# Kernel optimization log

Hardware: AMD Instinct MI355X
Metric: run time of the kernel (lower is better)

## Reference

```python
import jax, jax.numpy as jnp
import numpy as np

D_MODEL = 256
N_HEADS = 8
D_FF = 1024
N_LAYERS = 6
INPUT_DIM = 2
EPS = 1e-5  # torch LayerNorm default


def _layer_norm(x, g, b):
    m = jnp.mean(x, axis=-1, keepdims=True)
    v = jnp.mean((x - m) ** 2, axis=-1, keepdims=True)
    return (x - m) / jnp.sqrt(v + EPS) * g + b


def setup_inputs() -> dict:
    key = jax.random.key(0)
    ks = jax.random.split(key, 8)
    f32 = jnp.float32

    def w(k, shape, fan_in):
        return jax.random.normal(k, shape, f32) * (1.0 / np.sqrt(fan_in))

    return {
        "x": jax.random.normal(ks[0], (8, 1024, INPUT_DIM), f32),
        "in_w": w(ks[1], (INPUT_DIM, D_MODEL), INPUT_DIM),
        "in_b": jnp.zeros((D_MODEL,), f32),
        "ln1_g": jnp.ones((D_MODEL,), f32),
        "ln1_b": jnp.zeros((D_MODEL,), f32),
        "qkv_w": w(ks[2], (D_MODEL, 3 * D_MODEL), D_MODEL),
        "qkv_b": jnp.zeros((3 * D_MODEL,), f32),
        "out_w": w(ks[3], (D_MODEL, D_MODEL), D_MODEL),
        "out_b": jnp.zeros((D_MODEL,), f32),
        "lna_g": jnp.ones((D_MODEL,), f32),
        "lna_b": jnp.zeros((D_MODEL,), f32),
        "ln2_g": jnp.ones((D_MODEL,), f32),
        "ln2_b": jnp.zeros((D_MODEL,), f32),
        "ff1_w": w(ks[4], (D_MODEL, D_FF), D_MODEL),
        "ff1_b": jnp.zeros((D_FF,), f32),
        "ff2_w": w(ks[5], (D_FF, D_MODEL), D_FF),
        "ff2_b": jnp.zeros((D_MODEL,), f32),
        "lnf_g": jnp.ones((D_MODEL,), f32),
        "lnf_b": jnp.zeros((D_MODEL,), f32),
    }


def reference(x, in_w, in_b, ln1_g, ln1_b, qkv_w, qkv_b, out_w, out_b,
              lna_g, lna_b, ln2_g, ln2_b, ff1_w, ff1_b, ff2_w, ff2_b,
              lnf_g, lnf_b):
    B, L, _ = x.shape
    dk = D_MODEL // N_HEADS
    scale = 1.0 / np.sqrt(dk)
    top_k = max(1, L // 4)

    # sinusoidal positional encoding [L, D]
    pos = jnp.arange(L, dtype=jnp.float32)[:, None]
    div = jnp.exp(jnp.arange(0, D_MODEL, 2, dtype=jnp.float32)
                  * (-np.log(10000.0) / D_MODEL))
    pe = jnp.zeros((L, D_MODEL), jnp.float32)
    pe = pe.at[:, 0::2].set(jnp.sin(pos * div))
    pe = pe.at[:, 1::2].set(jnp.cos(pos * div))

    h = x @ in_w + in_b + pe[None]  # [B, L, D]

    # VoformerEncoder reuses the SAME layer object -> shared weights, 6 passes
    for _ in range(N_LAYERS):
        # --- self-attention sublayer (pre-norm) ---
        s2 = _layer_norm(h, ln1_g, ln1_b)
        qkv = (s2 @ qkv_w + qkv_b).reshape(B, L, 3, N_HEADS, dk)
        q = qkv[:, :, 0].transpose(0, 2, 1, 3)  # [B, H, L, dk]
        k = qkv[:, :, 1].transpose(0, 2, 1, 3)
        v = qkv[:, :, 2].transpose(0, 2, 1, 3)

        scores = jnp.einsum('bhqd,bhkd->bhqk', q, k) * scale  # [B,H,L,L]
        # ProbSparse: keep only the per-row top-k scores
        thr = jax.lax.top_k(scores, top_k)[0][..., -1:]
        sparse = jnp.where(scores >= thr, scores, -jnp.inf)
        attn = jax.nn.softmax(sparse, axis=-1)
        o = jnp.einsum('bhqk,bhkd->bhqd', attn, v)
        o = o.transpose(0, 2, 1, 3).reshape(B, L, D_MODEL)
        o = o @ out_w + out_b
        # InformerAttention applies its own residual + LayerNorm
        attn_out = _layer_norm(o + s2, lna_g, lna_b)
        h = h + attn_out

        # --- FFN sublayer with Volatilite activation ---
        s2 = _layer_norm(h, ln2_g, ln2_b)
        f = s2 @ ff1_w + ff1_b  # [B, L, d_ff]
        mean_f = jnp.mean(f, axis=1, keepdims=True)
        vol = jnp.sqrt(jnp.mean((mean_f - f) ** 2, axis=1, keepdims=True))
        f = f * vol
        f = f @ ff2_w + ff2_b
        h = h + f

    return _layer_norm(h, lnf_g, lnf_b)
```

## Files before the change

### kernel.cpp

```cpp
#include <hip/hip_runtime.h>
#include <math.h>

#define D_MODEL 256
#define NH 8
#define DFF 1024
#define NLAYERS 6
#define B_ 8
#define L_ 1024
#define NR (B_*L_)
#define TOPK 256
#define LNEPS 1e-5f

typedef __attribute__((ext_vector_type(8))) short bf16x8;
typedef __attribute__((ext_vector_type(4))) float f32x4;

__device__ __forceinline__ float wsum(float v){
  #pragma unroll
  for(int o=32;o>0;o>>=1) v += __shfl_xor(v,o,64);
  return v;
}
__device__ __forceinline__ float wmax(float v){
  #pragma unroll
  for(int o=32;o>0;o>>=1) v = fmaxf(v,__shfl_xor(v,o,64));
  return v;
}
__device__ __forceinline__ short f2bf(float x){
  unsigned u = __float_as_uint(x);
  u += 0x7fffu + ((u>>16)&1u);
  return (short)(u>>16);
}
__device__ __forceinline__ float bf2f(short s){
  return __uint_as_float(((unsigned)(unsigned short)s)<<16);
}
__device__ __forceinline__ void g2l(const short* g, short* l){
  __builtin_amdgcn_global_load_lds(
      (const __attribute__((address_space(1))) unsigned int*)g,
      (__attribute__((address_space(3))) unsigned int*)l,
      16, 0, 0);
}

__global__ __launch_bounds__(256) void embed_kernel(
    const float* __restrict__ x, const float* __restrict__ in_w,
    const float* __restrict__ in_b, float* __restrict__ h)
{
  int tid = blockIdx.x*256 + threadIdx.x;
  int n  = tid >> 6;
  int d0 = (tid & 63) << 2;
  int l  = n & (L_-1);
  float x0 = x[2*n], x1 = x[2*n+1];
  const float kf = -0.07195578415606394f;
  float pe[4];
  #pragma unroll
  for(int ii=0; ii<2; ++ii){
    int i = (d0>>1) + ii;
    float dv  = expf((float)i * kf);
    float ang = (float)l * dv;
    pe[2*ii]   = sinf(ang);
    pe[2*ii+1] = cosf(ang);
  }
  float4 w0 = *(const float4*)(in_w + d0);
  float4 w1 = *(const float4*)(in_w + D_MODEL + d0);
  float4 bb = *(const float4*)(in_b + d0);
  float4 o;
  o.x = x0*w0.x + x1*w1.x + bb.x + pe[0];
  o.y = x0*w0.y + x1*w1.y + bb.y + pe[1];
  o.z = x0*w0.z + x1*w1.z + bb.z + pe[2];
  o.w = x0*w0.w + x1*w1.w + bb.w + pe[3];
  *(float4*)(h + (size_t)n*D_MODEL + d0) = o;
}

__global__ __launch_bounds__(256) void wcvt(
    const float* __restrict__ W, short* __restrict__ WT, int N, int kshift)
{
  int idx = blockIdx.x*256 + threadIdx.x;
  int K = 1<<kshift;
  if (idx >= N*K) return;
  int n = idx >> kshift, k = idx & (K-1);
  WT[idx] = f2bf(W[(size_t)k*N + n]);
}

template<int OM>
__global__ __launch_bounds__(256) void ln_kernel(
    const float* __restrict__ in, const float* __restrict__ g,
    const float* __restrict__ b, float* __restrict__ out,
    short* __restrict__ outb)
{
  int wave = threadIdx.x >> 6, lane = threadIdx.x & 63;
  int row = blockIdx.x*4 + wave;
  float4 v = ((const float4*)(in + (size_t)row*D_MODEL))[lane];
  float s  = v.x+v.y+v.z+v.w;
  float sq = v.x*v.x+v.y*v.y+v.z*v.z+v.w*v.w;
  s = wsum(s); sq = wsum(sq);
  float mean = s*(1.f/D_MODEL);
  float var  = sq*(1.f/D_MODEL) - mean*mean;
  float rstd = 1.f/sqrtf(var + LNEPS);
  float4 gv = ((const float4*)g)[lane];
  float4 bv = ((const float4*)b)[lane];
  float4 o;
  o.x = (v.x-mean)*rstd*gv.x + bv.x;
  o.y = (v.y-mean)*rstd*gv.y + bv.y;
  o.z = (v.z-mean)*rstd*gv.z + bv.z;
  o.w = (v.w-mean)*rstd*gv.w + bv.w;
  if (OM == 0 || OM == 1){
    ((float4*)(out + (size_t)row*D_MODEL))[lane] = o;
  }
  if (OM == 3){
    float4* op = (float4*)(out + (size_t)row*D_MODEL) + lane;
    float4 hv = *op;
    o.x+=hv.x; o.y+=hv.y; o.z+=hv.z; o.w+=hv.w;
    *op = o;
  }
  if (OM == 1 || OM == 2){
    short4 s4; s4.x=f2bf(o.x); s4.y=f2bf(o.y); s4.z=f2bf(o.z); s4.w=f2bf(o.w);
    *(short4*)(outb + (size_t)row*D_MODEL + lane*4) = s4;
  }
}

template<int MODE>
__global__ __launch_bounds__(256) void mfma_gemm(
    const short* __restrict__ A, const short* __restrict__ BT,
    const float* __restrict__ bias, const float* __restrict__ resid,
    float* __restrict__ Cf, short* __restrict__ Cb, short* __restrict__ Vt,
    int N, int K)
{
  __shared__ __align__(16) short As[128*32];
  __shared__ __align__(16) short Bs[64*32];
  const int t = threadIdx.x, wv = t>>6, lane = t&63;
  const int r16 = lane&15, quad = lane>>4;
  const int m0 = blockIdx.y*128, n0 = blockIdx.x*64;
  const int ia0 = wv*128 + lane, ia1 = ia0 + 64;
  const int ib  = wv*64 + lane;
  const short* Ab = A  + (size_t)m0*K;
  const short* Bb = BT + (size_t)n0*K;
  const f32x4 z = {0.f,0.f,0.f,0.f};
  f32x4 acc[2][4];
  #pragma unroll
  for (int i=0;i<2;++i)
    #pragma unroll
    for (int j=0;j<4;++j) acc[i][j] = z;

  for (int k0 = 0; k0 < K; k0 += 32){
    __syncthreads();
    g2l(Ab + (size_t)(ia0>>2)*K + k0 + (ia0&3)*8, As + ia0*8);
    g2l(Ab + (size_t)(ia1>>2)*K + k0 + (ia1&3)*8, As + ia1*8);
    g2l(Bb + (size_t)(ib>>2)*K  + k0 + (ib&3)*8,  Bs + ib*8);
    __syncthreads();
    bf16x8 af0 = *(const bf16x8*)(As + ((wv*32      + r16)*32 + quad*8));
    bf16x8 af1 = *(const bf16x8*)(As + ((wv*32 + 16 + r16)*32 + quad*8));
    bf16x8 bf[4];
    #pragma unroll
    for (int ct=0; ct<4; ++ct)
      bf[ct] = *(const bf16x8*)(Bs + ((ct*16 + r16)*32 + quad*8));
    #pragma unroll
    for (int ct=0; ct<4; ++ct){
      acc[0][ct] = __builtin_amdgcn_mfma_f32_16x16x32_bf16(af0, bf[ct], acc[0][ct], 0,0,0);
      acc[1][ct] = __builtin_amdgcn_mfma_f32_16x16x32_bf16(af1, bf[ct], acc[1][ct], 0,0,0);
    }
  }

  #pragma unroll
  for (int rt=0; rt<2; ++rt){
    const int mb = m0 + wv*32 + rt*16 + quad*4;
    #pragma unroll
    for (int ct=0; ct<4; ++ct){
      const int n = n0 + ct*16 + r16;
      const float bv = bias[n];
      if (MODE == 0){
        if (n < 512){
          int region = n>>8, hh = (n>>5)&7, d = n&31;
          #pragma unroll
          for (int r=0;r<4;++r){
            int l = mb + r;
            size_t base = (((size_t)(region*64 + (l>>10)*8 + hh))*1024 + (l&1023))*32 + d;
            Cb[base] = f2bf(acc[rt][ct][r] + bv);
          }
        } else {
          int dv = n - 512, hh = dv>>5, d = dv&31;
          int b = mb>>10, lloc = mb&1023;
          size_t base = (((size_t)(b*8 + hh))*32 + d)*1024 + lloc;
          short4 s4;
          s4.x = f2bf(acc[rt][ct][0] + bv); s4.y = f2bf(acc[rt][ct][1] + bv);
          s4.z = f2bf(acc[rt][ct][2] + bv); s4.w = f2bf(acc[rt][ct][3] + bv);
          *(short4*)(Vt + base) = s4;
        }
      } else {
        #pragma unroll
        for (int r=0;r<4;++r){
          size_t off = (size_t)(mb + r)*N + n;
          float c = acc[rt][ct][r] + bv;
          if (MODE == 1) Cf[off] = c + resid[off];
          if (MODE == 2) Cb[off] = f2bf(c);
          if (MODE == 3) Cf[off] += c;
        }
      }
    }
  }
}

__global__ __launch_bounds__(256,4) void attn_mfma(
    const short* __restrict__ qkbf, const short* __restrict__ vT,
    short* __restrict__ ob)
{
  __shared__ __align__(16) short sc16[16*1024];
  const int t = threadIdx.x, wv = t>>6, lane = t&63;
  const int r16 = lane&15, quad = lane>>4;
  const int bh = blockIdx.x >> 6, qt = blockIdx.x & 63;

  bf16x8 aq = *(const bf16x8*)(qkbf + ((size_t)bh*1024 + qt*16 + r16)*32 + quad*8);
  const short* kb = qkbf + (size_t)(64 + bh)*1024*32;

  bf16x8 bk[16];
  #pragma unroll
  for (int tt=0; tt<16; ++tt)
    bk[tt] = *(const bf16x8*)(kb + (size_t)(wv*256 + tt*16 + r16)*32 + quad*8);
  #pragma unroll
  for (int tt=0; tt<16; ++tt){
    f32x4 c = {0.f,0.f,0.f,0.f};
    c = __builtin_amdgcn_mfma_f32_16x16x32_bf16(aq, bk[tt], c, 0, 0, 0);
    int key = wv*256 + tt*16 + r16;
    #pragma unroll
    for (int r=0;r<4;++r){
      int row = quad*4 + r;
      sc16[row*1024 + (key ^ ((row&7)<<3))] = f2bf(c[r]);
    }
  }
  __syncthreads();

  const float SC2 = 0.25500529485087056f;
  for (int rr=0; rr<4; ++rr){
    int row = wv*4 + rr;
    int s = (row&7)<<3;
    float scv[16]; int key[16];
    #pragma unroll
    for (int i=0;i<16;++i){
      short hsh = sc16[row*1024 + ((i*64+lane) ^ s)];
      scv[i] = bf2f(hsh);
      int u = (int)(unsigned short)hsh;
      key[i] = (u & 0x8000) ? (u ^ 0xFFFF) : (u | 0x8000);
    }
    int lo=0, hi=65536;
    while (hi - lo > 1){
      int mid = (lo+hi)>>1;
      int cnt = 0;
      #pragma unroll
      for (int i=0;i<16;++i)
        cnt += (int)__popcll(__ballot(key[i] >= mid));
      if (cnt >= TOPK) lo = mid; else hi = mid;
    }
    const int thr = lo;
    float mx = scv[0];
    #pragma unroll
    for (int i=1;i<16;++i) mx = fmaxf(mx, scv[i]);
    mx = wmax(mx);
    float sum = 0.f, w[16];
    #pragma unroll
    for (int i=0;i<16;++i){
      float e = (key[i] >= thr) ? exp2f((scv[i]-mx)*SC2) : 0.f;
      w[i] = e; sum += e;
    }
    sum = wsum(sum);
    const float inv = 1.f/sum;
    #pragma unroll
    for (int i=0;i<16;++i)
      sc16[row*1024 + ((i*64+lane) ^ s)] = f2bf(w[i]*inv);
  }
  __syncthreads();

  const short* vb = vT + (size_t)bh*32*1024;
  bf16x8 bvv[16];
  #pragma unroll
  for (int tt=0; tt<8; ++tt){
    int k0 = wv*256 + tt*32;
    #pragma unroll
    for (int n=0;n<2;++n)
      bvv[tt*2+n] = *(const bf16x8*)(vb + (size_t)(n*16 + r16)*1024 + k0 + quad*8);
  }
  f32x4 oa0 = {0.f,0.f,0.f,0.f}, oa1 = {0.f,0.f,0.f,0.f};
  #pragma unroll
  for (int tt=0; tt<8; ++tt){
    int k0 = wv*256 + tt*32;
    bf16x8 af = *(const bf16x8*)(sc16 + r16*1024 + ((k0 + quad*8) ^ ((r16&7)<<3)));
    oa0 = __builtin_amdgcn_mfma_f32_16x16x32_bf16(af, bvv[tt*2+0], oa0, 0, 0, 0);
    oa1 = __builtin_amdgcn_mfma_f32_16x16x32_bf16(af, bvv[tt*2+1], oa1, 0, 0, 0);
  }
  __syncthreads();
  float* po = (float*)sc16;
  #pragma unroll
  for (int r=0;r<4;++r){
    po[wv*512 + (quad*4+r)*32 +      r16] = oa0[r];
    po[wv*512 + (quad*4+r)*32 + 16 + r16] = oa1[r];
  }
  __syncthreads();
  int e = t*2;
  float v0 = po[e]   + po[512+e]   + po[1024+e]   + po[1536+e];
  float v1 = po[e+1] + po[512+e+1] + po[1024+e+1] + po[1536+e+1];
  int q = e>>5, d = e&31;
  int b = bh>>3, hh = bh&7;
  size_t off = ((size_t)(b*1024 + qt*16 + q))*256 + hh*32 + d;
  short2 s2o; s2o.x = f2bf(v0); s2o.y = f2bf(v1);
  *(short2*)(ob + off) = s2o;
}

__global__ __launch_bounds__(512) void vol_scale(short* __restrict__ f)
{
  __shared__ float ps[8][64], pq[8][64], vs[64];
  int b = blockIdx.x >> 4, cb = blockIdx.x & 15;
  int cl = threadIdx.x & 63, sl = threadIdx.x >> 6;
  int col = cb*64 + cl;
  short* fb = f + (size_t)b*L_*DFF + col;
  float s = 0.f, sq = 0.f;
  for (int l = sl*128; l < sl*128+128; ++l){
    float v = bf2f(fb[(size_t)l*DFF]);
    s += v; sq += v*v;
  }
  ps[sl][cl] = s; pq[sl][cl] = sq;
  __syncthreads();
  if (threadIdx.x < 64){
    float st=0.f, qt=0.f;
    #pragma unroll
    for (int i=0;i<8;++i){ st += ps[i][cl]; qt += pq[i][cl]; }
    float mean = st*(1.f/L_);
    float var  = qt*(1.f/L_) - mean*mean;
    vs[cl] = sqrtf(fmaxf(var, 0.f));
  }
  __syncthreads();
  float vv = vs[cl];
  for (int l = sl*128; l < sl*128+128; ++l){
    size_t o = (size_t)l*DFF;
    fb[o] = f2bf(bf2f(fb[o]) * vv);
  }
}

extern "C" void kernel_launch(void* const* d_in, const int* in_sizes, int n_in,
                              void* d_out, int out_size, void* d_ws, size_t ws_size,
                              hipStream_t stream) {
  const float* x     = (const float*)d_in[0];
  const float* in_w  = (const float*)d_in[1];
  const float* in_b  = (const float*)d_in[2];
  const float* ln1_g = (const float*)d_in[3];
  const float* ln1_b = (const float*)d_in[4];
  const float* qkv_w = (const float*)d_in[5];
  const float* qkv_b = (const float*)d_in[6];
  const float* out_w = (const float*)d_in[7];
  const float* out_b = (const float*)d_in[8];
  const float* lna_g = (const float*)d_in[9];
  const float* lna_b = (const float*)d_in[10];
  const float* ln2_g = (const float*)d_in[11];
  const float* ln2_b = (const float*)d_in[12];
  const float* ff1_w = (const float*)d_in[13];
  const float* ff1_b = (const float*)d_in[14];
  const float* ff2_w = (const float*)d_in[15];
  const float* ff2_b = (const float*)d_in[16];
  const float* lnf_g = (const float*)d_in[17];
  const float* lnf_b = (const float*)d_in[18];
  float* out = (float*)d_out;

  char* ws = (char*)d_ws;
  float* h     = (float*)(ws);
  float* s2    = (float*)(ws + (size_t)( 8<<20));
  short* s2b   = (short*)(ws + (size_t)(16<<20));
  short* qkbf  = (short*)(ws + (size_t)(20<<20));
  short* vTb   = (short*)(ws + (size_t)(28<<20));
  short* ob_b  = (short*)(ws + (size_t)(32<<20));
  short* f     = (short*)(ws + (size_t)(20<<20));
  float* tb    = (float*)(ws + (size_t)(36<<20));
  short* qkvwT = (short*)(ws + (size_t)(45<<20));
  short* outwT = (short*)(ws + (size_t)(45<<20) + 393216);
  short* ff1wT = (short*)(ws + (size_t)(45<<20) + 393216 + 131072);
  short* ff2wT = (short*)(ws + (size_t)(45<<20) + 393216 + 131072 + 524288);

  embed_kernel<<<NR*64/256, 256, 0, stream>>>(x, in_w, in_b, h);
  wcvt<<< 768, 256, 0, stream>>>(qkv_w, qkvwT,  768, 8);
  wcvt<<< 256, 256, 0, stream>>>(out_w, outwT,  256, 8);
  wcvt<<<1024, 256, 0, stream>>>(ff1_w, ff1wT, 1024, 8);
  wcvt<<<1024, 256, 0, stream>>>(ff2_w, ff2wT,  256, 10);

  for (int layer = 0; layer < NLAYERS; ++layer){
    ln_kernel<1><<<NR/4, 256, 0, stream>>>(h, ln1_g, ln1_b, s2, s2b);
    {
      dim3 g(768/64, NR/128);
      mfma_gemm<0><<<g, 256, 0, stream>>>(s2b, qkvwT, qkv_b, nullptr,
                                          nullptr, qkbf, vTb, 768, 256);
    }
    attn_mfma<<<64*64, 256, 0, stream>>>(qkbf, vTb, ob_b);
    {
      dim3 g(256/64, NR/128);
      mfma_gemm<1><<<g, 256, 0, stream>>>(ob_b, outwT, out_b, s2,
                                          tb, nullptr, nullptr, 256, 256);
    }
    ln_kernel<3><<<NR/4, 256, 0, stream>>>(tb, lna_g, lna_b, h, nullptr);
    ln_kernel<2><<<NR/4, 256, 0, stream>>>(h, ln2_g, ln2_b, nullptr, s2b);
    {
      dim3 g(1024/64, NR/128);
      mfma_gemm<2><<<g, 256, 0, stream>>>(s2b, ff1wT, ff1_b, nullptr,
                                          nullptr, f, nullptr, 1024, 256);
    }
    vol_scale<<<B_*16, 512, 0, stream>>>(f);
    {
      dim3 g(256/64, NR/128);
      mfma_gemm<3><<<g, 256, 0, stream>>>(f, ff2wT, ff2_b, nullptr,
                                          h, nullptr, nullptr, 256, 1024);
    }
  }
  ln_kernel<0><<<NR/4, 256, 0, stream>>>(h, lnf_g, lnf_b, out, nullptr);
}
```

Baseline: 1.362 ms.

## Fuse dual LayerNorms, bf16 residual, restructure attention top-k softmax

Fuses the post-attention LayerNorm, the residual add and the ln2 LayerNorm into one kernel, removing a full pass over h. The attention residual is now read from the bf16 s2b buffer instead of a separate fp32 s2 copy, which drops one fp32 write and read but loses some precision. The attention kernel processes two rows per wave with packed 32-bit LDS accesses and a new swizzle. It also bounds the binary search by the row maximum, defers softmax normalization to the output, and remaps block indices across heads.

```diff
diff --git a/kernel.cpp b/kernel.cpp
--- a/kernel.cpp
+++ b/kernel.cpp
@@ -19,11 +19,6 @@
   for(int o=32;o>0;o>>=1) v += __shfl_xor(v,o,64);
   return v;
 }
-__device__ __forceinline__ float wmax(float v){
-  #pragma unroll
-  for(int o=32;o>0;o>>=1) v = fmaxf(v,__shfl_xor(v,o,64));
-  return v;
-}
 __device__ __forceinline__ short f2bf(float x){
   unsigned u = __float_as_uint(x);
   u += 0x7fffu + ((u>>16)&1u);
@@ -31,6 +26,13 @@
 }
 __device__ __forceinline__ float bf2f(short s){
   return __uint_as_float(((unsigned)(unsigned short)s)<<16);
+}
+__device__ __forceinline__ int sortkey(unsigned u){
+  return (u & 0x8000u) ? (int)(u ^ 0xFFFFu) : (int)(u | 0x8000u);
+}
+__device__ __forceinline__ float kinvf(int k){
+  unsigned u = (k & 0x8000) ? ((unsigned)k ^ 0x8000u) : ((unsigned)k ^ 0xFFFFu);
+  return __uint_as_float(u << 16);
 }
 __device__ __forceinline__ void g2l(const short* g, short* l){
   __builtin_amdgcn_global_load_lds(
@@ -101,25 +103,60 @@
   o.y = (v.y-mean)*rstd*gv.y + bv.y;
   o.z = (v.z-mean)*rstd*gv.z + bv.z;
   o.w = (v.w-mean)*rstd*gv.w + bv.w;
-  if (OM == 0 || OM == 1){
+  if (OM == 0){
     ((float4*)(out + (size_t)row*D_MODEL))[lane] = o;
   }
-  if (OM == 3){
-    float4* op = (float4*)(out + (size_t)row*D_MODEL) + lane;
-    float4 hv = *op;
-    o.x+=hv.x; o.y+=hv.y; o.z+=hv.z; o.w+=hv.w;
-    *op = o;
-  }
-  if (OM == 1 || OM == 2){
+  if (OM == 2){
     short4 s4; s4.x=f2bf(o.x); s4.y=f2bf(o.y); s4.z=f2bf(o.z); s4.w=f2bf(o.w);
     *(short4*)(outb + (size_t)row*D_MODEL + lane*4) = s4;
   }
+}
+
+__global__ __launch_bounds__(256) void lnln_kernel(
+    const float* __restrict__ tb,
+    const float* __restrict__ ga, const float* __restrict__ ba,
+    const float* __restrict__ g2, const float* __restrict__ b2,
+    float* __restrict__ h, short* __restrict__ s2b)
+{
+  int wave = threadIdx.x >> 6, lane = threadIdx.x & 63;
+  int row = blockIdx.x*4 + wave;
+  float4 v = ((const float4*)(tb + (size_t)row*D_MODEL))[lane];
+  float s  = v.x+v.y+v.z+v.w;
+  float sq = v.x*v.x+v.y*v.y+v.z*v.z+v.w*v.w;
+  s = wsum(s); sq = wsum(sq);
+  float mean = s*(1.f/D_MODEL);
+  float var  = sq*(1.f/D_MODEL) - mean*mean;
+  float rstd = 1.f/sqrtf(var + LNEPS);
+  float4 gv = ((const float4*)ga)[lane];
+  float4 bv = ((const float4*)ba)[lane];
+  float4* hp = (float4*)(h + (size_t)row*D_MODEL) + lane;
+  float4 hv = *hp;
+  float4 hn;
+  hn.x = hv.x + (v.x-mean)*rstd*gv.x + bv.x;
+  hn.y = hv.y + (v.y-mean)*rstd*gv.y + bv.y;
+  hn.z = hv.z + (v.z-mean)*rstd*gv.z + bv.z;
+  hn.w = hv.w + (v.w-mean)*rstd*gv.w + bv.w;
+  *hp = hn;
+  float s2  = hn.x+hn.y+hn.z+hn.w;
+  float sq2 = hn.x*hn.x+hn.y*hn.y+hn.z*hn.z+hn.w*hn.w;
+  s2 = wsum(s2); sq2 = wsum(sq2);
+  float m2 = s2*(1.f/D_MODEL);
+  float v2 = sq2*(1.f/D_MODEL) - m2*m2;
+  float r2 = 1.f/sqrtf(v2 + LNEPS);
+  float4 g2v = ((const float4*)g2)[lane];
+  float4 b2v = ((const float4*)b2)[lane];
+  short4 s4;
+  s4.x = f2bf((hn.x-m2)*r2*g2v.x + b2v.x);
+  s4.y = f2bf((hn.y-m2)*r2*g2v.y + b2v.y);
+  s4.z = f2bf((hn.z-m2)*r2*g2v.z + b2v.z);
+  s4.w = f2bf((hn.w-m2)*r2*g2v.w + b2v.w);
+  *(short4*)(s2b + (size_t)row*D_MODEL + lane*4) = s4;
 }
 
 template<int MODE>
 __global__ __launch_bounds__(256) void mfma_gemm(
     const short* __restrict__ A, const short* __restrict__ BT,
-    const float* __restrict__ bias, const float* __restrict__ resid,
+    const float* __restrict__ bias, const short* __restrict__ residb,
     float* __restrict__ Cf, short* __restrict__ Cb, short* __restrict__ Vt,
     int N, int K)
 {
@@ -188,7 +225,7 @@
         for (int r=0;r<4;++r){
           size_t off = (size_t)(mb + r)*N + n;
           float c = acc[rt][ct][r] + bv;
-          if (MODE == 1) Cf[off] = c + resid[off];
+          if (MODE == 1) Cf[off] = c + bf2f(residb[off]);
           if (MODE == 2) Cb[off] = f2bf(c);
           if (MODE == 3) Cf[off] += c;
         }
@@ -202,9 +239,12 @@
     short* __restrict__ ob)
 {
   __shared__ __align__(16) short sc16[16*1024];
+  __shared__ float linv[16];
   const int t = threadIdx.x, wv = t>>6, lane = t&63;
   const int r16 = lane&15, quad = lane>>4;
-  const int bh = blockIdx.x >> 6, qt = blockIdx.x & 63;
+  const int blk = blockIdx.x;
+  const int bh = (blk & 7)*8 + ((blk>>3)&7);
+  const int qt = blk >> 6;
 
   bf16x8 aq = *(const bf16x8*)(qkbf + ((size_t)bh*1024 + qt*16 + r16)*32 + quad*8);
   const short* kb = qkbf + (size_t)(64 + bh)*1024*32;
@@ -217,52 +257,82 @@
   for (int tt=0; tt<16; ++tt){
     f32x4 c = {0.f,0.f,0.f,0.f};
     c = __builtin_amdgcn_mfma_f32_16x16x32_bf16(aq, bk[tt], c, 0, 0, 0);
-    int key = wv*256 + tt*16 + r16;
-    #pragma unroll
-    for (int r=0;r<4;++r){
-      int row = quad*4 + r;
-      sc16[row*1024 + (key ^ ((row&7)<<3))] = f2bf(c[r]);
-    }
+    const int pos = wv*256 + ((tt ^ quad)<<4) + r16;
+    #pragma unroll
+    for (int r=0;r<4;++r)
+      sc16[(quad*4+r)*1024 + pos] = f2bf(c[r]);
   }
   __syncthreads();
 
   const float SC2 = 0.25500529485087056f;
-  for (int rr=0; rr<4; ++rr){
-    int row = wv*4 + rr;
-    int s = (row&7)<<3;
-    float scv[16]; int key[16];
-    #pragma unroll
-    for (int i=0;i<16;++i){
-      short hsh = sc16[row*1024 + ((i*64+lane) ^ s)];
-      scv[i] = bf2f(hsh);
-      int u = (int)(unsigned short)hsh;
-      key[i] = (u & 0x8000) ? (u ^ 0xFFFF) : (u | 0x8000);
-    }
-    int lo=0, hi=65536;
-    while (hi - lo > 1){
-      int mid = (lo+hi)>>1;
-      int cnt = 0;
+  const int sw = wv << 4;
+  short* prow = sc16 + ((2*lane) ^ sw);
+  for (int rp=0; rp<2; ++rp){
+    const int ra = wv*4 + rp*2;
+    short* pa = prow + ra*1024;
+    short* pb = pa + 1024;
+    unsigned wa[8], wb[8];
+    #pragma unroll
+    for (int i=0;i<8;++i){
+      wa[i] = *(const unsigned*)(pa + i*128);
+      wb[i] = *(const unsigned*)(pb + i*128);
+    }
+    int ka[16], kb2[16];
+    #pragma unroll
+    for (int i=0;i<8;++i){
+      ka[2*i]    = sortkey(wa[i] & 0xFFFFu);
+      ka[2*i+1]  = sortkey(wa[i] >> 16);
+      kb2[2*i]   = sortkey(wb[i] & 0xFFFFu);
+      kb2[2*i+1] = sortkey(wb[i] >> 16);
+    }
+    int mxa = ka[0], mxb = kb2[0];
+    #pragma unroll
+    for (int i=1;i<16;++i){
+      mxa = (ka[i]  > mxa) ? ka[i]  : mxa;
+      mxb = (kb2[i] > mxb) ? kb2[i] : mxb;
+    }
+    #pragma unroll
+    for (int o=32;o>0;o>>=1){
+      int sa = __shfl_xor(mxa, o, 64); mxa = (sa > mxa) ? sa : mxa;
+      int sb = __shfl_xor(mxb, o, 64); mxb = (sb > mxb) ? sb : mxb;
+    }
+    int loA=0, hiA=mxa+1, loB=0, hiB=mxb+1;
+    while (hiA-loA > 1 || hiB-loB > 1){
+      int midA = (loA+hiA)>>1, midB = (loB+hiB)>>1;
+      int cA=0, cB=0;
       #pragma unroll
-      for (int i=0;i<16;++i)
-        cnt += (int)__popcll(__ballot(key[i] >= mid));
-      if (cnt >= TOPK) lo = mid; else hi = mid;
-    }
-    const int thr = lo;
-    float mx = scv[0];
-    #pragma unroll
-    for (int i=1;i<16;++i) mx = fmaxf(mx, scv[i]);
-    mx = wmax(mx);
-    float sum = 0.f, w[16];
-    #pragma unroll
-    for (int i=0;i<16;++i){
-      float e = (key[i] >= thr) ? exp2f((scv[i]-mx)*SC2) : 0.f;
-      w[i] = e; sum += e;
-    }
-    sum = wsum(sum);
-    const float inv = 1.f/sum;
-    #pragma unroll
-    for (int i=0;i<16;++i)
-      sc16[row*1024 + ((i*64+lane) ^ s)] = f2bf(w[i]*inv);
+      for (int i=0;i<16;++i){
+        cA += (int)__popcll(__ballot(ka[i]  >= midA));
+        cB += (int)__popcll(__ballot(kb2[i] >= midB));
+      }
+      if (cA >= TOPK) loA = midA; else hiA = midA;
+      if (cB >= TOPK) loB = midB; else hiB = midB;
+    }
+    const float thrA = kinvf(loA), thrB = kinvf(loB);
+    const float nmA = -kinvf(mxa)*SC2, nmB = -kinvf(mxb)*SC2;
+    float suma = 0.f, sumb = 0.f;
+    unsigned pka[8], pkb[8];
+    #pragma unroll
+    for (int i=0;i<8;++i){
+      float a0 = __uint_as_float(wa[i] << 16);
+      float a1 = __uint_as_float(wa[i] & 0xFFFF0000u);
+      float b0 = __uint_as_float(wb[i] << 16);
+      float b1 = __uint_as_float(wb[i] & 0xFFFF0000u);
+      float ea0 = (a0 >= thrA) ? exp2f(fmaf(a0, SC2, nmA)) : 0.f;
+      float ea1 = (a1 >= thrA) ? exp2f(fmaf(a1, SC2, nmA)) : 0.f;
+      float eb0 = (b0 >= thrB) ? exp2f(fmaf(b0, SC2, nmB)) : 0.f;
+      float eb1 = (b1 >= thrB) ? exp2f(fmaf(b1, SC2, nmB)) : 0.f;
+      suma += ea0 + ea1; sumb += eb0 + eb1;
+      pka[i] = (unsigned)(unsigned short)f2bf(ea0) | ((unsigned)(unsigned short)f2bf(ea1) << 16);
+      pkb[i] = (unsigned)(unsigned short)f2bf(eb0) | ((unsigned)(unsigned short)f2bf(eb1) << 16);
+    }
+    suma = wsum(suma); sumb = wsum(sumb);
+    if (lane == 0){ linv[ra] = 1.f/suma; linv[ra+1] = 1.f/sumb; }
+    #pragma unroll
+    for (int i=0;i<8;++i){
+      *(unsigned*)(pa + i*128) = pka[i];
+      *(unsigned*)(pb + i*128) = pkb[i];
+    }
   }
   __syncthreads();
 
@@ -275,11 +345,12 @@
     for (int n=0;n<2;++n)
       bvv[tt*2+n] = *(const bf16x8*)(vb + (size_t)(n*16 + r16)*1024 + k0 + quad*8);
   }
+  const int sA = ((r16>>2)&3) << 4;
   f32x4 oa0 = {0.f,0.f,0.f,0.f}, oa1 = {0.f,0.f,0.f,0.f};
   #pragma unroll
   for (int tt=0; tt<8; ++tt){
     int k0 = wv*256 + tt*32;
-    bf16x8 af = *(const bf16x8*)(sc16 + r16*1024 + ((k0 + quad*8) ^ ((r16&7)<<3)));
+    bf16x8 af = *(const bf16x8*)(sc16 + r16*1024 + ((k0 + quad*8) ^ sA));
     oa0 = __builtin_amdgcn_mfma_f32_16x16x32_bf16(af, bvv[tt*2+0], oa0, 0, 0, 0);
     oa1 = __builtin_amdgcn_mfma_f32_16x16x32_bf16(af, bvv[tt*2+1], oa1, 0, 0, 0);
   }
@@ -295,9 +366,10 @@
   float v0 = po[e]   + po[512+e]   + po[1024+e]   + po[1536+e];
   float v1 = po[e+1] + po[512+e+1] + po[1024+e+1] + po[1536+e+1];
   int q = e>>5, d = e&31;
+  const float inv = linv[q];
   int b = bh>>3, hh = bh&7;
   size_t off = ((size_t)(b*1024 + qt*16 + q))*256 + hh*32 + d;
-  short2 s2o; s2o.x = f2bf(v0); s2o.y = f2bf(v1);
+  short2 s2o; s2o.x = f2bf(v0*inv); s2o.y = f2bf(v1*inv);
   *(short2*)(ob + off) = s2o;
 }
 
@@ -357,17 +429,16 @@
 
   char* ws = (char*)d_ws;
   float* h     = (float*)(ws);
-  float* s2    = (float*)(ws + (size_t)( 8<<20));
-  short* s2b   = (short*)(ws + (size_t)(16<<20));
-  short* qkbf  = (short*)(ws + (size_t)(20<<20));
-  short* vTb   = (short*)(ws + (size_t)(28<<20));
-  short* ob_b  = (short*)(ws + (size_t)(32<<20));
-  short* f     = (short*)(ws + (size_t)(20<<20));
-  float* tb    = (float*)(ws + (size_t)(36<<20));
-  short* qkvwT = (short*)(ws + (size_t)(45<<20));
-  short* outwT = (short*)(ws + (size_t)(45<<20) + 393216);
-  short* ff1wT = (short*)(ws + (size_t)(45<<20) + 393216 + 131072);
-  short* ff2wT = (short*)(ws + (size_t)(45<<20) + 393216 + 131072 + 524288);
+  short* s2b   = (short*)(ws + (size_t)( 8<<20));
+  short* qkbf  = (short*)(ws + (size_t)(12<<20));
+  short* vTb   = (short*)(ws + (size_t)(20<<20));
+  short* ob_b  = (short*)(ws + (size_t)(24<<20));
+  short* f     = (short*)(ws + (size_t)(12<<20));
+  float* tb    = (float*)(ws + (size_t)(28<<20));
+  short* qkvwT = (short*)(ws + (size_t)(36<<20));
+  short* outwT = (short*)(ws + (size_t)(36<<20) + 393216);
+  short* ff1wT = (short*)(ws + (size_t)(36<<20) + 393216 + 131072);
+  short* ff2wT = (short*)(ws + (size_t)(36<<20) + 393216 + 131072 + 524288);
 
   embed_kernel<<<NR*64/256, 256, 0, stream>>>(x, in_w, in_b, h);
   wcvt<<< 768, 256, 0, stream>>>(qkv_w, qkvwT,  768, 8);
@@ -376,7 +447,7 @@
   wcvt<<<1024, 256, 0, stream>>>(ff2_w, ff2wT,  256, 10);
 
   for (int layer = 0; layer < NLAYERS; ++layer){
-    ln_kernel<1><<<NR/4, 256, 0, stream>>>(h, ln1_g, ln1_b, s2, s2b);
+    ln_kernel<2><<<NR/4, 256, 0, stream>>>(h, ln1_g, ln1_b, nullptr, s2b);
     {
       dim3 g(768/64, NR/128);
       mfma_gemm<0><<<g, 256, 0, stream>>>(s2b, qkvwT, qkv_b, nullptr,
@@ -385,11 +456,10 @@
     attn_mfma<<<64*64, 256, 0, stream>>>(qkbf, vTb, ob_b);
     {
       dim3 g(256/64, NR/128);
-      mfma_gemm<1><<<g, 256, 0, stream>>>(ob_b, outwT, out_b, s2,
+      mfma_gemm<1><<<g, 256, 0, stream>>>(ob_b, outwT, out_b, s2b,
                                           tb, nullptr, nullptr, 256, 256);
     }
-    ln_kernel<3><<<NR/4, 256, 0, stream>>>(tb, lna_g, lna_b, h, nullptr);
-    ln_kernel<2><<<NR/4, 256, 0, stream>>>(h, ln2_g, ln2_b, nullptr, s2b);
+    lnln_kernel<<<NR/4, 256, 0, stream>>>(tb, lna_g, lna_b, ln2_g, ln2_b, h, s2b);
     {
       dim3 g(1024/64, NR/128);
       mfma_gemm<2><<<g, 256, 0, stream>>>(s2b, ff1wT, ff1_b, nullptr,
```

After: 1.282 ms. 5.9% less time.
